# Kernel tuning notes

Hardware: AMD Instinct MI355X
Metric: run time of the kernel (lower is better)

The kernel has to match this reference:

```python
import jax, jax.numpy as jnp
import numpy as np

N = 100000   # num_nodes
E = 1600000  # num_edges (avg degree 16)
IN = 128     # input_dim
H = 4        # num_heads
D = 32       # hidden_dim per head (H*D == 128)
NEG_SLOPE = 0.2


def setup_inputs() -> dict:
    key = jax.random.key(0)
    ks = jax.random.split(key, 8)
    s = 0.1
    x = jax.random.normal(ks[0], (N, IN), jnp.float32)
    edge_index = jax.random.randint(ks[1], (2, E), 0, N, dtype=jnp.int32)
    W_gat = jax.random.normal(ks[2], (H * D, IN), jnp.float32) * s   # GATConv lin weight
    att_src = jax.random.normal(ks[3], (H, D), jnp.float32) * s
    att_dst = jax.random.normal(ks[4], (H, D), jnp.float32) * s
    bias_gat = jnp.zeros((H * D,), jnp.float32)
    W_lin = jax.random.normal(ks[5], (IN, H * D), jnp.float32) * s   # nn.Linear weight
    b_lin = jnp.zeros((IN,), jnp.float32)
    return {"x": x, "edge_index": edge_index, "W_gat": W_gat,
            "att_src": att_src, "att_dst": att_dst, "bias_gat": bias_gat,
            "W_lin": W_lin, "b_lin": b_lin}


def reference(x, edge_index, W_gat, att_src, att_dst, bias_gat, W_lin, b_lin):
    # (eval mode: all dropouts are identity; sparse edge weights unused in original)
    h = (x @ W_gat.T).reshape(N, H, D)                 # [N,H,D] per-head projections
    a_s = jnp.einsum('nhd,hd->nh', h, att_src)         # [N,H]
    a_d = jnp.einsum('nhd,hd->nh', h, att_dst)         # [N,H]
    # add self loops (PyG default)
    loop = jnp.arange(N, dtype=edge_index.dtype)
    src = jnp.concatenate([edge_index[0], loop])       # [E+N]
    dst = jnp.concatenate([edge_index[1], loop])       # [E+N]
    logits = jax.nn.leaky_relu(a_s[src] + a_d[dst], NEG_SLOPE)  # [E+N,H]
    # segment softmax over edges grouped by destination node
    m = jax.ops.segment_max(logits, dst, num_segments=N)        # [N,H]
    e = jnp.exp(logits - m[dst])
    denom = jax.ops.segment_sum(e, dst, num_segments=N)         # [N,H]
    alpha = e / denom[dst]                                      # [E+N,H]
    # scatter-aggregate weighted source features
    agg = jax.ops.segment_sum(alpha[:, :, None] * h[src], dst, num_segments=N)
    out = agg.reshape(N, H * D) + bias_gat             # concat heads + bias
    out = jax.nn.relu(out)
    return out @ W_lin.T + b_lin                       # [N, IN]
```

## Files before the change

### kernel.cpp

```cpp
#include <hip/hip_runtime.h>
#include <hip/hip_bf16.h>
#include <hip/hip_fp16.h>

#define NN 100000
#define EE 1600000
#define INF_DIM 128
#define NHEAD 4
#define HDIM 32
#define NEG_SLOPE 0.2f

#define GB 768

typedef __attribute__((ext_vector_type(8))) short short8;
typedef __attribute__((ext_vector_type(4))) float floatx4;

__device__ __forceinline__ unsigned int cvtpk_bf16(float lo, float hi) {
  unsigned int r;
  asm("v_cvt_pk_bf16_f32 %0, %1, %2" : "=v"(r) : "v"(lo), "v"(hi));
  return r;
}
__device__ __forceinline__ unsigned int packh2(float a, float b) {
  const __half ha = __float2half(a), hb = __float2half(b);
  const unsigned short ua = *(const unsigned short*)&ha;
  const unsigned short ub = *(const unsigned short*)&hb;
  return (unsigned int)ua | ((unsigned int)ub << 16);
}
__device__ __forceinline__ float pickw(const int4 e, const int head) {
  const unsigned int d = (head & 2) ? (unsigned int)e.z : (unsigned int)e.y;
  const unsigned short us =
      (head & 1) ? (unsigned short)(d >> 16) : (unsigned short)(d & 0xffffu);
  const __half h = *(const __half*)&us;
  return __half2float(h);
}
__device__ __forceinline__ void accum8h(const uint4 g, const float c,
                                        float* acc) {
  union { uint4 u; __half2 h[4]; } v;
  v.u = g;
#pragma unroll
  for (int j = 0; j < 4; ++j) {
    const float2 f = __half22float2(v.h[j]);
    acc[2 * j] = fmaf(c, f.x, acc[2 * j]);
    acc[2 * j + 1] = fmaf(c, f.y, acc[2 * j + 1]);
  }
}

#define LDA 136

__global__ __launch_bounds__(256) void gemm_mfma(
    const float* __restrict__ Af, const unsigned short* __restrict__ Ab,
    const float* __restrict__ W, const float* __restrict__ bias,
    unsigned short* __restrict__ Ch, float* __restrict__ Cf,
    const float* __restrict__ att_src, const float* __restrict__ att_dst,
    float* __restrict__ a_s, float* __restrict__ a_d,
    const int* __restrict__ dstE, int* __restrict__ deg8, int M) {
  __shared__ unsigned short sA[64 * LDA];
  __shared__ unsigned short sW[128 * LDA];
  const int tid = threadIdx.x;

  if (dstE) {
    int* mydeg = deg8 + (size_t)(blockIdx.x & 7) * NN;
    for (int e = blockIdx.x * 256 + tid; e < EE; e += GB * 256)
      atomicAdd(&mydeg[dstE[e]], 1);
  }

  {
    const int r = tid >> 1;
    const int c0 = (tid & 1) * 64;
#pragma unroll
    for (int j = 0; j < 16; ++j) {
      const float4 v = *(const float4*)&W[r * 128 + c0 + j * 4];
      uint2 u;
      u.x = cvtpk_bf16(v.x, v.y);
      u.y = cvtpk_bf16(v.z, v.w);
      *(uint2*)&sW[r * LDA + c0 + j * 4] = u;
    }
  }

  const int wv = tid >> 6;
  const int lane = tid & 63;
  const int l16 = lane & 15;
  const int quad = lane >> 4;
  const int ntiles = (M + 63) >> 6;

  float avs[8], avd[8];
  if (a_s) {
#pragma unroll
    for (int nt = 0; nt < 8; ++nt) {
      avs[nt] = att_src[nt * 16 + l16];
      avd[nt] = att_dst[nt * 16 + l16];
    }
  }

  for (int t = blockIdx.x; t < ntiles; t += GB) {
    const int m0 = t * 64;
    __syncthreads();
    {
      const int r = tid >> 2;
      const int gm = m0 + r;
      const int c0 = (tid & 3) * 32;
      if (gm < M) {
        if (Af) {
#pragma unroll
          for (int j = 0; j < 8; ++j) {
            const float4 v = *(const float4*)&Af[(size_t)gm * 128 + c0 + j * 4];
            uint2 u;
            u.x = cvtpk_bf16(v.x, v.y);
            u.y = cvtpk_bf16(v.z, v.w);
            *(uint2*)&sA[r * LDA + c0 + j * 4] = u;
          }
        } else {
#pragma unroll
          for (int j = 0; j < 4; ++j) {
            const uint4 v = *(const uint4*)&Ab[(size_t)gm * 128 + c0 + j * 8];
            *(uint4*)&sA[r * LDA + c0 + j * 8] = v;
          }
        }
      } else {
#pragma unroll
        for (int j = 0; j < 4; ++j) {
          uint4 z;
          z.x = z.y = z.z = z.w = 0u;
          *(uint4*)&sA[r * LDA + c0 + j * 8] = z;
        }
      }
    }
    __syncthreads();

    floatx4 acc[8];
#pragma unroll
    for (int i = 0; i < 8; ++i) acc[i] = (floatx4){0.f, 0.f, 0.f, 0.f};

    const unsigned short* aRow = &sA[(wv * 16 + l16) * LDA + quad * 8];
#pragma unroll
    for (int kc = 0; kc < 4; ++kc) {
      const short8 afrag = *(const short8*)(aRow + kc * 32);
#pragma unroll
      for (int nt = 0; nt < 8; ++nt) {
        const short8 bfrag =
            *(const short8*)&sW[(nt * 16 + l16) * LDA + kc * 32 + quad * 8];
        acc[nt] = __builtin_amdgcn_mfma_f32_16x16x32_bf16(afrag, bfrag,
                                                          acc[nt], 0, 0, 0);
      }
    }

    const int mrow = m0 + wv * 16 + quad * 4;
#pragma unroll
    for (int nt = 0; nt < 8; ++nt) {
      const int col = nt * 16 + l16;
      const float bv = Cf ? bias[col] : 0.f;
#pragma unroll
      for (int r = 0; r < 4; ++r) {
        const int gm = mrow + r;
        if (gm < M) {
          const float v = acc[nt][r];
          if (Ch) {
            const __half hh = __float2half(v);
            Ch[(size_t)gm * 128 + col] = *(const unsigned short*)&hh;
          } else {
            Cf[(size_t)gm * 128 + col] = v + bv;
          }
        }
      }
    }

    if (a_s) {
#pragma unroll
      for (int r = 0; r < 4; ++r) {
        float ps0 = acc[0][r] * avs[0] + acc[1][r] * avs[1];
        float ps1 = acc[2][r] * avs[2] + acc[3][r] * avs[3];
        float ps2 = acc[4][r] * avs[4] + acc[5][r] * avs[5];
        float ps3 = acc[6][r] * avs[6] + acc[7][r] * avs[7];
        float pd0 = acc[0][r] * avd[0] + acc[1][r] * avd[1];
        float pd1 = acc[2][r] * avd[2] + acc[3][r] * avd[3];
        float pd2 = acc[4][r] * avd[4] + acc[5][r] * avd[5];
        float pd3 = acc[6][r] * avd[6] + acc[7][r] * avd[7];
#pragma unroll
        for (int off = 1; off < 16; off <<= 1) {
          ps0 += __shfl_xor(ps0, off);
          ps1 += __shfl_xor(ps1, off);
          ps2 += __shfl_xor(ps2, off);
          ps3 += __shfl_xor(ps3, off);
          pd0 += __shfl_xor(pd0, off);
          pd1 += __shfl_xor(pd1, off);
          pd2 += __shfl_xor(pd2, off);
          pd3 += __shfl_xor(pd3, off);
        }
        const int gm = mrow + r;
        if (gm < M) {
          const int hs = l16 & 3;
          float vs = ps0;
          if (hs == 1) vs = ps1;
          if (hs == 2) vs = ps2;
          if (hs == 3) vs = ps3;
          float vd = pd0;
          if (hs == 1) vd = pd1;
          if (hs == 2) vd = pd2;
          if (hs == 3) vd = pd3;
          if (l16 < 4)
            a_s[gm * 4 + hs] = vs;
          else if (l16 < 8)
            a_d[gm * 4 + hs] = vd;
        }
      }
    }
  }
}

__global__ __launch_bounds__(256) void alloc_kernel(
    const int* __restrict__ deg8, int* __restrict__ deg,
    int* __restrict__ rowptr, int* __restrict__ cur,
    int* __restrict__ counter) {
  const int i = blockIdx.x * blockDim.x + threadIdx.x;
  const int lane = threadIdx.x & 63;
  int d = 0;
  if (i < NN) {
#pragma unroll
    for (int k = 0; k < 8; ++k) d += deg8[(size_t)k * NN + i];
  }
  int s = d;
#pragma unroll
  for (int off = 1; off < 64; off <<= 1) {
    const int v = __shfl_up(s, off, 64);
    if (lane >= off) s += v;
  }
  const int total = __shfl(s, 63, 64);
  int base = 0;
  if (lane == 63) base = atomicAdd(counter, total);
  base = __shfl(base, 63, 64);
  const int p = base + s - d;
  if (i < NN) {
    rowptr[i] = p;
    cur[i] = p;
    deg[i] = d;
  }
}

__global__ void scatter_kernel(const int* __restrict__ src,
                               const int* __restrict__ dst,
                               const float* __restrict__ a_s,
                               const float* __restrict__ a_d,
                               int* __restrict__ cur, int4* __restrict__ ebuf) {
  const int iA = blockIdx.x * blockDim.x + threadIdx.x;
  const int iB = iA + (EE / 2);
  const int sA_ = src[iA];
  const int dA = dst[iA];
  const int sB_ = src[iB];
  const int dB = dst[iB];
  const int pA = atomicAdd(&cur[dA], 1);
  const int pB = atomicAdd(&cur[dB], 1);
  const float4 asA = *(const float4*)&a_s[sA_ * 4];
  const float4 adA = *(const float4*)&a_d[dA * 4];
  const float4 asB = *(const float4*)&a_s[sB_ * 4];
  const float4 adB = *(const float4*)&a_d[dB * 4];
  float4 lA, lB;
  lA.x = asA.x + adA.x;
  lA.y = asA.y + adA.y;
  lA.z = asA.z + adA.z;
  lA.w = asA.w + adA.w;
  lB.x = asB.x + adB.x;
  lB.y = asB.y + adB.y;
  lB.z = asB.z + adB.z;
  lB.w = asB.w + adB.w;
  lA.x = lA.x > 0.f ? lA.x : NEG_SLOPE * lA.x;
  lA.y = lA.y > 0.f ? lA.y : NEG_SLOPE * lA.y;
  lA.z = lA.z > 0.f ? lA.z : NEG_SLOPE * lA.z;
  lA.w = lA.w > 0.f ? lA.w : NEG_SLOPE * lA.w;
  lB.x = lB.x > 0.f ? lB.x : NEG_SLOPE * lB.x;
  lB.y = lB.y > 0.f ? lB.y : NEG_SLOPE * lB.y;
  lB.z = lB.z > 0.f ? lB.z : NEG_SLOPE * lB.z;
  lB.w = lB.w > 0.f ? lB.w : NEG_SLOPE * lB.w;
  int4 eA, eB;
  eA.x = sA_;
  eA.y = (int)packh2(__expf(lA.x), __expf(lA.y));
  eA.z = (int)packh2(__expf(lA.z), __expf(lA.w));
  eA.w = 0;
  eB.x = sB_;
  eB.y = (int)packh2(__expf(lB.x), __expf(lB.y));
  eB.z = (int)packh2(__expf(lB.z), __expf(lB.w));
  eB.w = 0;
  ebuf[pA] = eA;
  ebuf[pB] = eB;
}

__global__ __launch_bounds__(256) void aggregate_kernel(
    const uint4* __restrict__ hbd4, const float* __restrict__ a_s,
    const float* __restrict__ a_d, const float* __restrict__ bias_gat,
    const int* __restrict__ rowptr, const int* __restrict__ deg,
    const int4* __restrict__ ebuf, uint4* __restrict__ obd4) {
  const int wave = (blockIdx.x * blockDim.x + threadIdx.x) >> 6;
  if (wave >= NN) return;
  const int lane = threadIdx.x & 63;
  const int q = lane >> 4;
  const int f = lane & 15;
  const int head = f >> 2;
  const int n = wave;

  float acc[8];
  float ds;
  {
    const float l0 = a_s[n * 4 + head] + a_d[n * 4 + head];
    const float l = fmaxf(l0, NEG_SLOPE * l0);
    float cs = __expf(l);
    if (q != 0) cs = 0.f;
    union { uint4 u; __half2 h[4]; } v;
    v.u = hbd4[(size_t)n * 16 + f];
#pragma unroll
    for (int j = 0; j < 4; ++j) {
      const float2 fv = __half22float2(v.h[j]);
      acc[2 * j] = cs * fv.x;
      acc[2 * j + 1] = cs * fv.y;
    }
    ds = cs;
  }

  const int beg = rowptr[n];
  const int end = beg + deg[n];
  for (int i = beg; i < end; i += 16) {
    int4 e0, e1, e2, e3;
    {
      const int i0 = i + q, i1 = i + 4 + q, i2 = i + 8 + q, i3 = i + 12 + q;
      e0 = ebuf[i0 < end ? i0 : end - 1];
      e1 = ebuf[i1 < end ? i1 : end - 1];
      e2 = ebuf[i2 < end ? i2 : end - 1];
      e3 = ebuf[i3 < end ? i3 : end - 1];
    }
    const uint4 g0 = hbd4[(size_t)e0.x * 16 + f];
    const uint4 g1 = hbd4[(size_t)e1.x * 16 + f];
    const uint4 g2 = hbd4[(size_t)e2.x * 16 + f];
    const uint4 g3 = hbd4[(size_t)e3.x * 16 + f];
    float c0 = pickw(e0, head);
    float c1 = pickw(e1, head);
    float c2 = pickw(e2, head);
    float c3 = pickw(e3, head);
    if (i + q >= end) c0 = 0.f;
    if (i + 4 + q >= end) c1 = 0.f;
    if (i + 8 + q >= end) c2 = 0.f;
    if (i + 12 + q >= end) c3 = 0.f;
    accum8h(g0, c0, acc);
    accum8h(g1, c1, acc);
    accum8h(g2, c2, acc);
    accum8h(g3, c3, acc);
    ds += c0 + c1 + c2 + c3;
  }

#pragma unroll
  for (int j = 0; j < 8; ++j) {
    acc[j] += __shfl_xor(acc[j], 16);
    acc[j] += __shfl_xor(acc[j], 32);
  }
  ds += __shfl_xor(ds, 16);
  ds += __shfl_xor(ds, 32);

  if (q == 0) {
    const float inv = 1.0f / ds;
    const float4 b0 = *(const float4*)&bias_gat[f * 8];
    const float4 b1 = *(const float4*)&bias_gat[f * 8 + 4];
    float v0 = acc[0] * inv + b0.x;
    float v1 = acc[1] * inv + b0.y;
    float v2 = acc[2] * inv + b0.z;
    float v3 = acc[3] * inv + b0.w;
    float v4 = acc[4] * inv + b1.x;
    float v5 = acc[5] * inv + b1.y;
    float v6 = acc[6] * inv + b1.z;
    float v7 = acc[7] * inv + b1.w;
    v0 = v0 > 0.f ? v0 : 0.f;
    v1 = v1 > 0.f ? v1 : 0.f;
    v2 = v2 > 0.f ? v2 : 0.f;
    v3 = v3 > 0.f ? v3 : 0.f;
    v4 = v4 > 0.f ? v4 : 0.f;
    v5 = v5 > 0.f ? v5 : 0.f;
    v6 = v6 > 0.f ? v6 : 0.f;
    v7 = v7 > 0.f ? v7 : 0.f;
    uint4 r;
    r.x = cvtpk_bf16(v0, v1);
    r.y = cvtpk_bf16(v2, v3);
    r.z = cvtpk_bf16(v4, v5);
    r.w = cvtpk_bf16(v6, v7);
    obd4[(size_t)n * 16 + f] = r;
  }
}

extern "C" void kernel_launch(void* const* d_in, const int* in_sizes, int n_in,
                              void* d_out, int out_size, void* d_ws,
                              size_t ws_size, hipStream_t stream) {
  const float* x = (const float*)d_in[0];
  const int* ei = (const int*)d_in[1];
  const float* W_gat = (const float*)d_in[2];
  const float* att_src = (const float*)d_in[3];
  const float* att_dst = (const float*)d_in[4];
  const float* bias_gat = (const float*)d_in[5];
  const float* W_lin = (const float*)d_in[6];
  const float* b_lin = (const float*)d_in[7];
  float* out = (float*)d_out;

  char* ws = (char*)d_ws;
  size_t off = 0;
  unsigned short* hb = (unsigned short*)(ws + off);
  off += (size_t)NN * 128 * 2;
  unsigned short* ob = (unsigned short*)(ws + off);
  off += (size_t)NN * 128 * 2;
  float* a_s = (float*)(ws + off); off += (size_t)NN * 4 * 4;
  float* a_d = (float*)(ws + off); off += (size_t)NN * 4 * 4;
  int* deg8 = (int*)(ws + off); off += (size_t)8 * NN * 4;
  int* deg = (int*)(ws + off); off += (size_t)NN * 4;
  int* rowptr = (int*)(ws + off); off += (size_t)(NN + 4) * 4;
  int* cur = (int*)(ws + off); off += (size_t)NN * 4;
  int* counter = (int*)(ws + off); off += 16;
  int4* ebuf = (int4*)(ws + off); off += (size_t)EE * 16;

  const int* src = ei;
  const int* dst = ei + EE;

  hipMemsetAsync(deg8, 0, (size_t)8 * NN * 4, stream);
  hipMemsetAsync(counter, 0, 16, stream);
  gemm_mfma<<<GB, 256, 0, stream>>>(x, nullptr, W_gat, nullptr, hb, nullptr,
                                    att_src, att_dst, a_s, a_d, dst, deg8, NN);
  alloc_kernel<<<(NN + 255) / 256, 256, 0, stream>>>(deg8, deg, rowptr, cur,
                                                     counter);
  scatter_kernel<<<(EE / 2 + 255) / 256, 256, 0, stream>>>(src, dst, a_s, a_d,
                                                           cur, ebuf);
  aggregate_kernel<<<(NN + 3) / 4, 256, 0, stream>>>(
      (const uint4*)hb, a_s, a_d, bias_gat, rowptr, deg, ebuf,
      (uint4*)ob);
  gemm_mfma<<<GB, 256, 0, stream>>>(nullptr, ob, W_lin, b_lin, nullptr, out,
                                    nullptr, nullptr, nullptr, nullptr,
                                    nullptr, nullptr, NN);
}
```

Before: 385.3 us.

## Load GEMM A fragments directly from global into registers, drop LDS staging

The GEMM kernel no longer stages the A tile through shared memory. Each lane now loads its MFMA A fragment straight from global memory, converting fp32 to bf16 in registers. Rows past the end are clamped to M-1, and per-tile __syncthreads barriers are removed so only the one-time W load is synchronized. The grid stride grows from 768 to 1024 blocks, which also changes the degree-counting atomic loop's stride. This cuts LDS traffic and barriers and lowers shared memory per block, which may raise occupancy, but global loads become narrower and less coalesced per lane.

```diff
diff --git a/kernel.cpp b/kernel.cpp
--- a/kernel.cpp
+++ b/kernel.cpp
@@ -9,7 +9,7 @@
 #define HDIM 32
 #define NEG_SLOPE 0.2f
 
-#define GB 768
+#define GB 1024
 
 typedef __attribute__((ext_vector_type(8))) short short8;
 typedef __attribute__((ext_vector_type(4))) float floatx4;
@@ -53,7 +53,6 @@
     const float* __restrict__ att_src, const float* __restrict__ att_dst,
     float* __restrict__ a_s, float* __restrict__ a_d,
     const int* __restrict__ dstE, int* __restrict__ deg8, int M) {
-  __shared__ unsigned short sA[64 * LDA];
   __shared__ unsigned short sW[128 * LDA];
   const int tid = threadIdx.x;
 
@@ -75,6 +74,7 @@
       *(uint2*)&sW[r * LDA + c0 + j * 4] = u;
     }
   }
+  __syncthreads();
 
   const int wv = tid >> 6;
   const int lane = tid & 63;
@@ -91,54 +91,43 @@
     }
   }
 
+  const unsigned short* wBase = &sW[l16 * LDA + quad * 8];
+
   for (int t = blockIdx.x; t < ntiles; t += GB) {
     const int m0 = t * 64;
-    __syncthreads();
-    {
-      const int r = tid >> 2;
-      const int gm = m0 + r;
-      const int c0 = (tid & 3) * 32;
-      if (gm < M) {
-        if (Af) {
-#pragma unroll
-          for (int j = 0; j < 8; ++j) {
-            const float4 v = *(const float4*)&Af[(size_t)gm * 128 + c0 + j * 4];
-            uint2 u;
-            u.x = cvtpk_bf16(v.x, v.y);
-            u.y = cvtpk_bf16(v.z, v.w);
-            *(uint2*)&sA[r * LDA + c0 + j * 4] = u;
-          }
-        } else {
-#pragma unroll
-          for (int j = 0; j < 4; ++j) {
-            const uint4 v = *(const uint4*)&Ab[(size_t)gm * 128 + c0 + j * 8];
-            *(uint4*)&sA[r * LDA + c0 + j * 8] = v;
-          }
-        }
-      } else {
-#pragma unroll
-        for (int j = 0; j < 4; ++j) {
-          uint4 z;
-          z.x = z.y = z.z = z.w = 0u;
-          *(uint4*)&sA[r * LDA + c0 + j * 8] = z;
-        }
+    const int arow = m0 + wv * 16 + l16;
+    const int arowc = arow < M ? arow : M - 1;
+
+    short8 af[4];
+    if (Af) {
+      const float* ap = &Af[(size_t)arowc * 128 + quad * 8];
+#pragma unroll
+      for (int kc = 0; kc < 4; ++kc) {
+        const float4 v0 = *(const float4*)(ap + kc * 32);
+        const float4 v1 = *(const float4*)(ap + kc * 32 + 4);
+        union { uint4 u; short8 s; } c;
+        c.u.x = cvtpk_bf16(v0.x, v0.y);
+        c.u.y = cvtpk_bf16(v0.z, v0.w);
+        c.u.z = cvtpk_bf16(v1.x, v1.y);
+        c.u.w = cvtpk_bf16(v1.z, v1.w);
+        af[kc] = c.s;
       }
-    }
-    __syncthreads();
+    } else {
+      const unsigned short* ap = &Ab[(size_t)arowc * 128 + quad * 8];
+#pragma unroll
+      for (int kc = 0; kc < 4; ++kc) af[kc] = *(const short8*)(ap + kc * 32);
+    }
 
     floatx4 acc[8];
 #pragma unroll
     for (int i = 0; i < 8; ++i) acc[i] = (floatx4){0.f, 0.f, 0.f, 0.f};
 
-    const unsigned short* aRow = &sA[(wv * 16 + l16) * LDA + quad * 8];
 #pragma unroll
     for (int kc = 0; kc < 4; ++kc) {
-      const short8 afrag = *(const short8*)(aRow + kc * 32);
 #pragma unroll
       for (int nt = 0; nt < 8; ++nt) {
-        const short8 bfrag =
-            *(const short8*)&sW[(nt * 16 + l16) * LDA + kc * 32 + quad * 8];
-        acc[nt] = __builtin_amdgcn_mfma_f32_16x16x32_bf16(afrag, bfrag,
+        const short8 bfrag = *(const short8*)(wBase + nt * 16 * LDA + kc * 32);
+        acc[nt] = __builtin_amdgcn_mfma_f32_16x16x32_bf16(af[kc], bfrag,
                                                           acc[nt], 0, 0, 0);
       }
     }
```

Result: no change. 381.4 us (-1.0%).
